# Performance work log

Hardware: AMD Instinct MI355X
Metric: run time of the kernel (lower is better)

Reference implementation:

```python
import jax, jax.numpy as jnp
import numpy as np

BATCH = 16384
EMBED = 128
HEAD_VOCAB = 100000
TAIL_VOCAB = 1000000
NUM_NEG = 100


def setup_inputs() -> dict:
    key = jax.random.key(0)
    k1, k2, k3, k4, k5, k6, k7 = jax.random.split(key, 7)
    initrange = 0.5 / EMBED
    return {
        "head_table": jax.random.uniform(k1, (HEAD_VOCAB + 1, EMBED), jnp.float32, -initrange, initrange),
        "tail_table": jax.random.uniform(k2, (TAIL_VOCAB + 1, EMBED), jnp.float32, -initrange, initrange),
        "relation_vec": jax.random.uniform(k3, (1, EMBED), jnp.float32, -initrange, initrange),
        "bias_table": jax.random.normal(k4, (TAIL_VOCAB + 1,), jnp.float32) * 0.01,
        "head_idxs": jax.random.randint(k5, (BATCH,), 0, HEAD_VOCAB),
        "tail_idxs": jax.random.randint(k6, (BATCH,), 0, TAIL_VOCAB),
        "neg_idxs": jax.random.randint(k7, (NUM_NEG,), 0, TAIL_VOCAB),  # stands in for multinomial(distrib)
    }


def reference(head_table, tail_table, relation_vec, bias_table, head_idxs, tail_idxs, neg_idxs):
    # Embedding gathers
    head_vec = head_table[head_idxs]          # [B, D]
    tail_vec = tail_table[tail_idxs]          # [B, D]
    rel_bias = bias_table[tail_idxs]          # [B]
    neg_vec = tail_table[neg_idxs]            # [K, D]

    example_vec = head_vec + relation_vec     # [B, D] (relation_vec broadcasts from [1, D])

    # Positive logits: per-row dot product + bias
    pos_logits = jnp.einsum("bd,bd->b", tail_vec, example_vec) + rel_bias   # [B]
    pos_loss = -jax.nn.log_sigmoid(pos_logits)                              # [B]

    # Negative logits: shared negative set, mm + broadcast bias
    neg_logits = jnp.einsum("bd,kd->bk", example_vec, neg_vec) + rel_bias[:, None]  # [B, K]
    neg_loss = jnp.sum(-jax.nn.log_sigmoid(-neg_logits), axis=1)                    # [B]

    loss = jnp.mean(pos_loss + neg_loss)
    return loss
```

## Files before the change

kernel.cpp:

```cpp
#include <hip/hip_runtime.h>
#include <math.h>

#define BATCH     16384
#define EMBED     128
#define NUM_NEG   100
#define ROWS_PB   64
#define NBLOCKS   (BATCH / ROWS_PB)
#define KG        4
#define KPT       (NUM_NEG / KG)
#define D4        (EMBED / 4)

__device__ __forceinline__ float softplus(float x) {
    return fmaxf(x, 0.0f) + log1pf(expf(-fabsf(x)));
}

__global__ __launch_bounds__(256) void ke_main(
    const float* __restrict__ head_table,
    const float* __restrict__ tail_table,
    const float* __restrict__ relation_vec,
    const float* __restrict__ bias_table,
    const int*   __restrict__ head_idxs,
    const int*   __restrict__ tail_idxs,
    const int*   __restrict__ neg_idxs,
    float*       __restrict__ partials)
{
    __shared__ float4 neg_lds[NUM_NEG * D4];
    __shared__ float4 rel_lds[D4];
    __shared__ float  wsum[KG];

    const int t = threadIdx.x;

    for (int i = t; i < NUM_NEG * D4; i += 256) {
        const int k  = i >> 5;
        const int d4 = i & 31;
        const float4* src = (const float4*)(tail_table + (size_t)neg_idxs[k] * EMBED);
        neg_lds[i] = src[d4];
    }
    if (t < D4) rel_lds[t] = ((const float4*)relation_vec)[t];
    __syncthreads();

    const int r   = t & 63;
    const int kg  = t >> 6;
    const int row = blockIdx.x * ROWS_PB + r;

    const int   hidx = head_idxs[row];
    const int   tidx = tail_idxs[row];
    const float bias = bias_table[tidx];
    const float4* hrow = (const float4*)(head_table + (size_t)hidx * EMBED);
    const float4* trow = (const float4*)(tail_table + (size_t)tidx * EMBED);

    float acc[KPT];
    #pragma unroll
    for (int i = 0; i < KPT; ++i) acc[i] = 0.0f;
    float pos = 0.0f;

    const int kbase = kg * KPT;

    for (int d4 = 0; d4 < D4; ++d4) {
        const float4 h  = hrow[d4];
        const float4 rv = rel_lds[d4];
        const float4 e  = make_float4(h.x + rv.x, h.y + rv.y,
                                      h.z + rv.z, h.w + rv.w);
        if (kg == 0) {
            const float4 tv = trow[d4];
            pos = fmaf(e.x, tv.x, fmaf(e.y, tv.y, fmaf(e.z, tv.z, fmaf(e.w, tv.w, pos))));
        }
        #pragma unroll
        for (int kk = 0; kk < KPT; ++kk) {
            const float4 n = neg_lds[(kbase + kk) * D4 + d4];
            acc[kk] = fmaf(e.x, n.x, fmaf(e.y, n.y, fmaf(e.z, n.z, fmaf(e.w, n.w, acc[kk]))));
        }
    }

    float local = 0.0f;
    #pragma unroll
    for (int kk = 0; kk < KPT; ++kk)
        local += softplus(acc[kk] + bias);
    if (kg == 0)
        local += softplus(-(pos + bias));

    #pragma unroll
    for (int off = 32; off; off >>= 1)
        local += __shfl_down(local, off, 64);
    if ((t & 63) == 0) wsum[kg] = local;
    __syncthreads();
    if (t == 0)
        partials[blockIdx.x] = wsum[0] + wsum[1] + wsum[2] + wsum[3];
}

__global__ __launch_bounds__(256) void ke_reduce(
    const float* __restrict__ partials, float* __restrict__ out)
{
    __shared__ float wsum[4];
    const int t = threadIdx.x;
    float v = partials[t];
    #pragma unroll
    for (int off = 32; off; off >>= 1)
        v += __shfl_down(v, off, 64);
    if ((t & 63) == 0) wsum[t >> 6] = v;
    __syncthreads();
    if (t == 0)
        out[0] = (wsum[0] + wsum[1] + wsum[2] + wsum[3]) * (1.0f / (float)BATCH);
}

extern "C" void kernel_launch(void* const* d_in, const int* in_sizes, int n_in,
                              void* d_out, int out_size, void* d_ws, size_t ws_size,
                              hipStream_t stream)
{
    const float* head_table   = (const float*)d_in[0];
    const float* tail_table   = (const float*)d_in[1];
    const float* relation_vec = (const float*)d_in[2];
    const float* bias_table   = (const float*)d_in[3];
    const int*   head_idxs    = (const int*)d_in[4];
    const int*   tail_idxs    = (const int*)d_in[5];
    const int*   neg_idxs     = (const int*)d_in[6];
    float*       out          = (float*)d_out;
    float*       partials     = (float*)d_ws;

    ke_main<<<NBLOCKS, 256, 0, stream>>>(head_table, tail_table, relation_vec,
                                         bias_table, head_idxs, tail_idxs,
                                         neg_idxs, partials);
    ke_reduce<<<1, 256, 0, stream>>>(partials, out);
}
```

Measured before the change: 607.1 us.

## Stage head+relation rows in LDS and split negatives across eight waves

Head rows plus relation vector are gathered once per block into padded LDS instead of each of the four waves re-reading the head row from global memory. The block grows to 512 threads: seven waves cover 13 negatives each, and the eighth covers the last 9 negatives plus the positive dot product. This removes the redundant global head reads and the kg==0 branch inside the inner loop, and puts more waves on each block. In exchange it uses more LDS per block (about 84 KB), which may limit how many blocks fit on a CU.

```diff
diff --git a/kernel.cpp b/kernel.cpp
--- a/kernel.cpp
+++ b/kernel.cpp
@@ -6,15 +6,20 @@
 #define NUM_NEG   100
 #define ROWS_PB   64
 #define NBLOCKS   (BATCH / ROWS_PB)
-#define KG        4
-#define KPT       (NUM_NEG / KG)
+#define THREADS   512
 #define D4        (EMBED / 4)
+#define KPT       13
+#define KPT_LAST  9
 
 __device__ __forceinline__ float softplus(float x) {
     return fmaxf(x, 0.0f) + log1pf(expf(-fabsf(x)));
 }
 
-__global__ __launch_bounds__(256) void ke_main(
+__device__ __forceinline__ float fma4(const float4 a, const float4 b, float c) {
+    return fmaf(a.x, b.x, fmaf(a.y, b.y, fmaf(a.z, b.z, fmaf(a.w, b.w, c))));
+}
+
+__global__ __launch_bounds__(THREADS) void ke_main(
     const float* __restrict__ head_table,
     const float* __restrict__ tail_table,
     const float* __restrict__ relation_vec,
@@ -25,67 +30,81 @@
     float*       __restrict__ partials)
 {
     __shared__ float4 neg_lds[NUM_NEG * D4];
-    __shared__ float4 rel_lds[D4];
-    __shared__ float  wsum[KG];
+    __shared__ float4 e_lds[ROWS_PB * 33];
+    __shared__ float  wsum[8];
 
-    const int t = threadIdx.x;
+    const int t        = threadIdx.x;
+    const int base_row = blockIdx.x * ROWS_PB;
 
-    for (int i = t; i < NUM_NEG * D4; i += 256) {
+    for (int i = t; i < NUM_NEG * D4; i += THREADS) {
         const int k  = i >> 5;
         const int d4 = i & 31;
-        const float4* src = (const float4*)(tail_table + (size_t)neg_idxs[k] * EMBED);
-        neg_lds[i] = src[d4];
+        neg_lds[i] = ((const float4*)(tail_table + (size_t)neg_idxs[k] * EMBED))[d4];
     }
-    if (t < D4) rel_lds[t] = ((const float4*)relation_vec)[t];
+    for (int i = t; i < ROWS_PB * D4; i += THREADS) {
+        const int row = i >> 5;
+        const int d4  = i & 31;
+        const float4 h  = ((const float4*)(head_table +
+                           (size_t)head_idxs[base_row + row] * EMBED))[d4];
+        const float4 rv = ((const float4*)relation_vec)[d4];
+        e_lds[row * 33 + d4] = make_float4(h.x + rv.x, h.y + rv.y,
+                                           h.z + rv.z, h.w + rv.w);
+    }
     __syncthreads();
 
     const int r   = t & 63;
     const int kg  = t >> 6;
-    const int row = blockIdx.x * ROWS_PB + r;
+    const int row = base_row + r;
 
-    const int   hidx = head_idxs[row];
     const int   tidx = tail_idxs[row];
     const float bias = bias_table[tidx];
-    const float4* hrow = (const float4*)(head_table + (size_t)hidx * EMBED);
-    const float4* trow = (const float4*)(tail_table + (size_t)tidx * EMBED);
 
     float acc[KPT];
     #pragma unroll
     for (int i = 0; i < KPT; ++i) acc[i] = 0.0f;
     float pos = 0.0f;
 
-    const int kbase = kg * KPT;
+    float local = 0.0f;
 
-    for (int d4 = 0; d4 < D4; ++d4) {
-        const float4 h  = hrow[d4];
-        const float4 rv = rel_lds[d4];
-        const float4 e  = make_float4(h.x + rv.x, h.y + rv.y,
-                                      h.z + rv.z, h.w + rv.w);
-        if (kg == 0) {
-            const float4 tv = trow[d4];
-            pos = fmaf(e.x, tv.x, fmaf(e.y, tv.y, fmaf(e.z, tv.z, fmaf(e.w, tv.w, pos))));
+    if (kg < 7) {
+        const int kbase = kg * KPT;
+        #pragma unroll 4
+        for (int d4 = 0; d4 < D4; ++d4) {
+            const float4 e = e_lds[r * 33 + d4];
+            #pragma unroll
+            for (int kk = 0; kk < KPT; ++kk)
+                acc[kk] = fma4(e, neg_lds[(kbase + kk) * D4 + d4], acc[kk]);
         }
         #pragma unroll
-        for (int kk = 0; kk < KPT; ++kk) {
-            const float4 n = neg_lds[(kbase + kk) * D4 + d4];
-            acc[kk] = fmaf(e.x, n.x, fmaf(e.y, n.y, fmaf(e.z, n.z, fmaf(e.w, n.w, acc[kk]))));
+        for (int kk = 0; kk < KPT; ++kk)
+            local += softplus(acc[kk] + bias);
+    } else {
+        const float4* trow = (const float4*)(tail_table + (size_t)tidx * EMBED);
+        #pragma unroll 4
+        for (int d4 = 0; d4 < D4; ++d4) {
+            const float4 e  = e_lds[r * 33 + d4];
+            pos = fma4(e, trow[d4], pos);
+            #pragma unroll
+            for (int kk = 0; kk < KPT_LAST; ++kk)
+                acc[kk] = fma4(e, neg_lds[(91 + kk) * D4 + d4], acc[kk]);
         }
+        #pragma unroll
+        for (int kk = 0; kk < KPT_LAST; ++kk)
+            local += softplus(acc[kk] + bias);
+        local += softplus(-(pos + bias));
     }
-
-    float local = 0.0f;
-    #pragma unroll
-    for (int kk = 0; kk < KPT; ++kk)
-        local += softplus(acc[kk] + bias);
-    if (kg == 0)
-        local += softplus(-(pos + bias));
 
     #pragma unroll
     for (int off = 32; off; off >>= 1)
         local += __shfl_down(local, off, 64);
     if ((t & 63) == 0) wsum[kg] = local;
     __syncthreads();
-    if (t == 0)
-        partials[blockIdx.x] = wsum[0] + wsum[1] + wsum[2] + wsum[3];
+    if (t == 0) {
+        float s = 0.0f;
+        #pragma unroll
+        for (int w = 0; w < 8; ++w) s += wsum[w];
+        partials[blockIdx.x] = s;
+    }
 }
 
 __global__ __launch_bounds__(256) void ke_reduce(
@@ -117,8 +136,8 @@
     float*       out          = (float*)d_out;
     float*       partials     = (float*)d_ws;
 
-    ke_main<<<NBLOCKS, 256, 0, stream>>>(head_table, tail_table, relation_vec,
-                                         bias_table, head_idxs, tail_idxs,
-                                         neg_idxs, partials);
+    ke_main<<<NBLOCKS, THREADS, 0, stream>>>(head_table, tail_table, relation_vec,
+                                             bias_table, head_idxs, tail_idxs,
+                                             neg_idxs, partials);
     ke_reduce<<<1, 256, 0, stream>>>(partials, out);
 }
```

Result: faster. 587.6 us (-3.2%).
